# Kernel tuning notes

Measured on AMD Instinct MI355X. Metric: run time of the kernel, lower is better.

Reference implementation:

```python
import jax, jax.numpy as jnp
import numpy as np

C_LOGIT = 10.0  # logit clipping constant C from __init__
NEG_INF = -1e8


def setup_inputs() -> dict:
    key = jax.random.key(0)
    ks = jax.random.split(key, 10)
    B, S, E, H = 512, 256, 128, 128
    u = lambda k, sh: jax.random.uniform(k, sh, jnp.float32, -0.1, 0.1)
    return {
        "low_context_vector": jax.random.normal(ks[0], (B, S, E), jnp.float32),
        "original_node": jax.random.uniform(ks[1], (S, 2), jnp.float32),
        "mask": jnp.zeros((B, S), jnp.float32),
        # learned parameters
        "low_init_w": jax.random.uniform(ks[2], (2 * E,), jnp.float32, -1.0, 1.0),
        "Wc": u(ks[3], (E, E)),   "bc": u(ks[4], (E,)),     # low_h_context_embed
        "Wv": u(ks[5], (2 * E, E)), "bv": u(ks[6], (E,)),   # low_v_weight_embed
        "Wq": u(ks[7], (E, H)),                              # pointer query proj
        "Wref": u(ks[8], (E, H)),                            # pointer ref proj
        "v": u(ks[9], (H,)),                                 # pointer score vector
    }


def _decode(cv, mask, low_init_w, Wc, bc, Wv, bv, Wq, Wref, v, key):
    B, S, E = cv.shape
    h_bar = jnp.mean(cv, axis=1) @ Wc + bc              # [B,E]
    rest0 = low_init_w @ Wv + bv                        # [E]
    query0 = h_bar + rest0[None, :]                     # [B,E]
    ref = cv @ Wref                                     # [B,S,H], hoisted out of loop
    mask = mask.at[:, 0].set(1.0)                       # start node visited
    keys = jax.random.split(key, S - 1)
    binds = jnp.arange(B)

    def step(carry, k):
        mask, query, init_h, i = carry
        u_ = jnp.tanh((query @ Wq)[:, None, :] + ref) @ v      # [B,S]
        logits = jnp.where(mask > 0, NEG_INF, C_LOGIT * jnp.tanh(u_))
        logp = jax.nn.log_softmax(logits, axis=-1)
        g = jax.random.gumbel(k, logits.shape, logits.dtype)
        idx = jnp.argmax(logits + g, axis=-1)                  # Categorical sample, [B]
        lp = jnp.take_along_axis(logp, idx[:, None], axis=1)[:, 0]
        mask = mask.at[binds, idx].set(1.0)
        h = cv[binds, idx]                                     # gathered embedding [B,E]
        init_h = jnp.where(i == 0, h, init_h)                  # first pick cached
        query = h_bar + (jnp.concatenate([init_h, h], axis=-1) @ Wv + bv)
        return (mask, query, init_h, i + 1), (idx, lp)

    init = (mask, query0, jnp.zeros((B, E), cv.dtype), jnp.int32(0))
    _, (idxs, lps) = jax.lax.scan(step, init, keys)
    return idxs.T, lps.T  # [B, S-1] each


def reference(low_context_vector, original_node, mask, low_init_w, Wc, bc, Wv, bv, Wq, Wref, v):
    # original_node only feeds a printed local_reward in the torch code; it does
    # not affect the returned (indices, log_probs), so it is unused here.
    return _decode(low_context_vector, mask, low_init_w, Wc, bc, Wv, bv, Wq, Wref, v,
                   jax.random.key(42))
```

## Files before the change

### kernel.cpp

```cpp
#include <hip/hip_runtime.h>
#include <hip/hip_bf16.h>
#include <stdint.h>
#include <math.h>

#define NBATCH 512
#define NS 256
#define NE 128
#define NH 128
#define NSTEPS 255
#define NEGINF -1e8f
#define SENT_NEG -1e30f

__device__ __forceinline__ uint32_t rotl32(uint32_t x, uint32_t r) {
  return (x << r) | (x >> (32u - r));
}

__device__ __forceinline__ void tf2x32(uint32_t k0, uint32_t k1,
                                       uint32_t x0, uint32_t x1,
                                       uint32_t& o0, uint32_t& o1) {
  uint32_t ks2 = k0 ^ k1 ^ 0x1BD11BDAu;
  x0 += k0; x1 += k1;
#define TF_R4(a,b,c,d) \
  x0 += x1; x1 = rotl32(x1,a); x1 ^= x0; \
  x0 += x1; x1 = rotl32(x1,b); x1 ^= x0; \
  x0 += x1; x1 = rotl32(x1,c); x1 ^= x0; \
  x0 += x1; x1 = rotl32(x1,d); x1 ^= x0;
  TF_R4(13,15,26,6)   x0 += k1;  x1 += ks2 + 1u;
  TF_R4(17,29,16,24)  x0 += ks2; x1 += k0 + 2u;
  TF_R4(13,15,26,6)   x0 += k0;  x1 += k1 + 3u;
  TF_R4(17,29,16,24)  x0 += k1;  x1 += ks2 + 4u;
  TF_R4(13,15,26,6)   x0 += ks2; x1 += k0 + 5u;
#undef TF_R4
  o0 = x0; o1 = x1;
}

__device__ __forceinline__ float gumbel_of(uint2 key, uint32_t j) {
  uint32_t o0, o1;
  tf2x32(key.x, key.y, 0u, j, o0, o1);
  uint32_t bits = o0 ^ o1;
  float f = __uint_as_float((bits >> 9) | 0x3f800000u) - 1.0f;
  float u = (f == 0.0f) ? 1.17549435e-38f : f;
  float l1 = -logf(u);
  return -logf(l1);
}

__device__ __forceinline__ float nr_tanh(float x) {
  const float Chi = 2.8853900432586670f;
  const float Clo = 3.8519259822379735e-08f;
  float m = fmaf(x, Chi, x * Clo);
  m = fminf(m, 126.0f);
  float tt = __builtin_amdgcn_exp2f(m);
  float d  = tt + 1.0f;
  float r  = __builtin_amdgcn_rcpf(d);
  r = r * fmaf(-d, r, 2.0f);
  return fmaf(-2.0f, r, 1.0f);
}

__device__ __forceinline__ double dot32(const float4* __restrict__ a,
                                        const float4* __restrict__ bp) {
  double s = 0.0;
#pragma unroll
  for (int q = 0; q < 8; ++q) {
    float4 x = a[q], y = bp[q];
    s += (double)x.x * (double)y.x + (double)x.y * (double)y.y
       + (double)x.z * (double)y.z + (double)x.w * (double)y.w;
  }
  return s;
}

__device__ __forceinline__ double dot4d(float4 a, float4 b) {
  return ((double)a.x * (double)b.x + (double)a.y * (double)b.y)
       + ((double)a.z * (double)b.z + (double)a.w * (double)b.w);
}

__global__ void k1_mats(const float* __restrict__ Wv, const float* __restrict__ Wq,
                        const float* __restrict__ liw, const float* __restrict__ bvv,
                        float* __restrict__ M1T, float* __restrict__ M2T,
                        float* __restrict__ rest0) {
  int e = blockIdx.x, h = threadIdx.x;
  __shared__ float wrow[NE];
  if (e < 256) {
    wrow[h] = Wv[e * NE + h];
    __syncthreads();
    double a = 0.0;
    for (int k = 0; k < NE; ++k) a += (double)wrow[k] * (double)Wq[k * NH + h];
    if (e < 128) M1T[h * NE + e] = (float)a;
    else         M2T[h * NE + (e - 128)] = (float)a;
  } else {
    double a = 0.0;
    for (int k = 0; k < 2 * NE; ++k) a += (double)liw[k] * (double)Wv[k * NE + h];
    rest0[h] = (float)a + bvv[h];
  }
}

__global__ void k2_base(const float* __restrict__ cv, const float* __restrict__ Wc,
                        const float* __restrict__ bc, const float* __restrict__ bvv,
                        const float* __restrict__ Wq, const float* __restrict__ rest0,
                        double* __restrict__ qqbase, float* __restrict__ qq0) {
  int b = blockIdx.x, h = threadIdx.x;
  int b256 = b << 8;
  __shared__ float meanL[NE], hbarL[NE];
  double ms = 0.0;
  for (int s = 0; s < NS; ++s) ms += (double)cv[((size_t)b256 + s) * NE + h];
  meanL[h] = (float)(ms * (1.0 / 256.0));
  __syncthreads();
  double a = 0.0;
  for (int e = 0; e < NE; ++e) a += (double)meanL[e] * (double)Wc[e * NE + h];
  hbarL[h] = (float)a + bc[h];
  __syncthreads();
  double ab = 0.0, a0 = 0.0;
  for (int k = 0; k < NE; ++k) {
    double w = (double)Wq[k * NH + h];
    ab += (double)(hbarL[k] + bvv[k]) * w;
    a0 += (double)(hbarL[k] + rest0[k]) * w;
  }
  qqbase[(size_t)b * NH + h] = ab;
  qq0[(size_t)b * NH + h] = (float)a0;
}

__global__ __launch_bounds__(256, 4)
void k_a2v3(const float* __restrict__ cv, const float* __restrict__ M2T,
            double* __restrict__ A2) {
  const int b  = blockIdx.x >> 3;
  const int s0 = (blockIdx.x & 7) << 5;
  const int t  = threadIdx.x;
  const int h  = t >> 1;
  const int kh = t & 1;
  const int b256 = b << 8;
  __shared__ float cvS[32][132];
  for (int idx = t; idx < 32 * NE; idx += 256) {
    int r = idx >> 7, c = idx & 127;
    cvS[r][c] = cv[((size_t)(b256 + s0 + r)) * NE + c];
  }
  __syncthreads();
  float4 m2r[16];
  {
    const float4* m2p = (const float4*)(M2T + (size_t)h * NE + kh * 64);
#pragma unroll
    for (int q = 0; q < 16; ++q) m2r[q] = m2p[q];
  }
#pragma unroll 2
  for (int sLoc = 0; sLoc < 32; ++sLoc) {
    const float4* cr4 = ((const float4*)&cvS[sLoc][0]) + kh * 16;
    double c0 = 0.0, c1 = 0.0;
#pragma unroll
    for (int q = 0; q < 16; q += 2) {
      c0 += dot4d(cr4[q],     m2r[q]);
      c1 += dot4d(cr4[q + 1], m2r[q + 1]);
    }
    double s = c0 + c1;
    s += __shfl_xor(s, 1, 64);
    if (kh == 0)
      A2[((size_t)(b256 + s0 + sLoc)) * NH + h] = s;
  }
}

struct MainSh {
  alignas(16) float  qq[NH];
  alignas(16) float  vvf[NH];
  alignas(8)  double partA[NS];
  float  logitArr[NS];
  alignas(8)  double base128[NH];
  uint2  keyL[NSTEPS];
  float  redV[8];
  float  redS[8];
  int    redI[8];
};

struct PreSh {
  float cvS[NS][33];
  float wS[32][NH];
};

template <int MODE>
__global__ __launch_bounds__(512, 4)
void decode_main(const float* __restrict__ cv,
                 const float* __restrict__ mask_in,
                 const float* __restrict__ Wref,
                 const float* __restrict__ vvec,
                 const double* __restrict__ qqbase,
                 const float* __restrict__ M1T,
                 const float* __restrict__ M2T,
                 const float* __restrict__ qq0,
                 const double* __restrict__ A2,
                 float* __restrict__ out) {
  const int b = blockIdx.x;
  const int t = threadIdx.x;
  const int b256 = b << 8;
  const int chunk = (((t >> 6) & 3) + b) & 3;
  const int i = (chunk << 6) | (t & 63);
  const int halfo = t >> 8;
  const int hb = halfo << 6;

  __shared__ union { PreSh pre; MainSh m; } sh;
  __shared__ short rowIdA[NS], rowIdB[NS], posA[NS], posB[NS];
  __shared__ int nActSh[2], jSh[2], tmp8[4];
  __shared__ alignas(16) float refScratch[NE];

  bool act0 = false;
  if (t < NS) {
    act0 = !((t == 0) || (mask_in[(size_t)b256 + t] > 0.0f));
    uint64_t mb = __ballot(act0);
    int lane = t & 63, w = t >> 6;
    int pre = __popcll(mb & (((uint64_t)1 << lane) - 1));
    if (lane == 0) tmp8[w] = (int)__popcll(mb);
    posA[t] = (short)pre;
  }
  __syncthreads();
  if (t < NS) {
    int base = 0;
    for (int k = 0; k < (t >> 6); ++k) base += tmp8[k];
    int p = base + (int)posA[t];
    if (act0) rowIdA[p] = (short)t;
    posA[t] = (short)p;
  }
  if (t == 0) {
    nActSh[0] = tmp8[0] + tmp8[1] + tmp8[2] + tmp8[3];
    jSh[0] = -1;
  }
  __syncthreads();
  const int nAct0 = nActSh[0];

  const int myRow0 = (i < nAct0) ? (int)rowIdA[i] : 0;
  float refr[64];
#pragma unroll
  for (int j = 0; j < 64; ++j) refr[j] = 0.0f;

  for (int ec = 0; ec < 4; ++ec) {
    __syncthreads();
    for (int ii = t; ii < 32 * NH; ii += 512) {
      int r = ii >> 7, c = ii & 127;
      sh.pre.wS[r][c] = Wref[(ec * 32 + r) * NH + c];
    }
    for (int ii = t; ii < NS * 32; ii += 512) {
      int r = ii >> 5, c = ii & 31;
      sh.pre.cvS[r][c] = cv[((size_t)b256 + r) * NE + ec * 32 + c];
    }
    __syncthreads();
    for (int hc = 0; hc < 8; ++hc) {
      double a[8] = {0,0,0,0,0,0,0,0};
      for (int e = 0; e < 32; ++e) {
        double cd = (double)sh.pre.cvS[myRow0][e];
        const float* wp = &sh.pre.wS[e][hb + hc * 8];
#pragma unroll
        for (int j = 0; j < 8; ++j) a[j] += cd * (double)wp[j];
      }
#pragma unroll
      for (int j = 0; j < 8; ++j) refr[hc * 8 + j] += (float)a[j];
    }
  }
  __syncthreads();

  if (t < NSTEPS) {
    uint32_t o0, o1;
    tf2x32(0u, 42u, 0u, (uint32_t)t, o0, o1);
    sh.m.keyL[t] = make_uint2(o0, o1);
  }
  if (t < NH) {
    sh.m.vvf[t] = vvec[t];
    sh.m.qq[t] = qq0[(size_t)b * NH + t];
  }
  __syncthreads();

  float g = 0.0f;
  if (halfo && i < nAct0)
    g = gumbel_of(sh.m.keyL[0], (uint32_t)(b256 + myRow0));

  for (int step = 0; step < NSTEPS; ++step) {
    const int cur = step & 1;
    const short* rowId_c = cur ? rowIdB : rowIdA;
    const short* pos_c   = cur ? posB   : posA;
    short* rowId_n = cur ? rowIdA : rowIdB;
    short* pos_n   = cur ? posA   : posB;
    const int nA    = nActSh[cur];
    const int jPrev = jSh[cur];
    const bool active = (i < nA);
    const int myRow = active ? (int)rowId_c[i] : 0;

    if (jPrev >= 0 && i == jPrev) {
      const float4* rs4 = (const float4*)(refScratch + hb);
#pragma unroll
      for (int q = 0; q < 16; ++q) {
        float4 v4 = rs4[q];
        refr[4 * q + 0] = v4.x; refr[4 * q + 1] = v4.y;
        refr[4 * q + 2] = v4.z; refr[4 * q + 3] = v4.w;
      }
    }

    double accH = 0.0;
    if (active) {
      double a0 = 0, a1 = 0, a2 = 0, a3 = 0;
      const float4* qq4 = (const float4*)(sh.m.qq + hb);
      const float4* vv4 = (const float4*)(sh.m.vvf + hb);
#pragma unroll
      for (int q = 0; q < 16; ++q) {
        float4 qv = qq4[q];
        float4 wv = vv4[q];
        a0 += (double)nr_tanh(qv.x + refr[4 * q + 0]) * (double)wv.x;
        a1 += (double)nr_tanh(qv.y + refr[4 * q + 1]) * (double)wv.y;
        a2 += (double)nr_tanh(qv.z + refr[4 * q + 2]) * (double)wv.z;
        a3 += (double)nr_tanh(qv.w + refr[4 * q + 3]) * (double)wv.w;
      }
      accH = (a0 + a1) + (a2 + a3);
      if (!halfo) sh.m.partA[i] = accH;
    }
    __syncthreads();

    if (halfo) {
      float val = SENT_NEG; int vRow = 0x7fffffff; float term = 0.0f;
      if (active) {
        float u_ = (float)(sh.m.partA[i] + accH);
        float logit = 10.0f * (float)tanh((double)u_);
        sh.m.logitArr[myRow] = logit;
        term = expf(logit);
        val = logit + g;
        vRow = myRow;
      }
      float bvv = val; int bR = vRow; float bss = term;
#pragma unroll
      for (int mm = 1; mm <= 32; mm <<= 1) {
        float ov = __shfl_xor(bvv, mm, 64);
        int   oR = __shfl_xor(bR,  mm, 64);
        float os = __shfl_xor(bss, mm, 64);
        bss += os;
        if (ov > bvv || (ov == bvv && oR < bR)) { bvv = ov; bR = oR; }
      }
      if ((t & 63) == 0) {
        int w = t >> 6;
        sh.m.redV[w] = bvv; sh.m.redI[w] = bR; sh.m.redS[w] = bss;
      }
    }
    __syncthreads();

    float BV = sh.m.redV[4]; int BR = sh.m.redI[4];
#pragma unroll
    for (int k = 5; k < 8; ++k) {
      float ov = sh.m.redV[k]; int oR = sh.m.redI[k];
      if (ov > BV || (ov == BV && oR < BR)) { BV = ov; BR = oR; }
    }
    if ((unsigned)BR > 255u) BR = 0;
    const int BI = BR;
    const int jj = (int)pos_c[BI];

    double a2v = 0.0;
    if (MODE == 1 && step > 0 && step + 1 < NSTEPS && t < NH)
      a2v = A2[(size_t)(b256 + BI) * NH + t];

    if (t == 0) {
      float SS = (sh.m.redS[4] + sh.m.redS[5]) + (sh.m.redS[6] + sh.m.redS[7]);
      float lp = sh.m.logitArr[BI] - (float)log((double)SS);
      out[(size_t)b * NSTEPS + step] = (float)BI;
      out[(size_t)NBATCH * NSTEPS + (size_t)b * NSTEPS + step] = lp;
      nActSh[cur ^ 1] = nA - 1;
      jSh[cur ^ 1] = (jj < nA - 1) ? jj : -1;
    }

    if (t < NS) {
      int donorRow = (int)rowId_c[nA - 1];
      short rid = (t == jj) ? (short)donorRow : rowId_c[t];
      rowId_n[t] = rid;
      if (t < nA - 1) pos_n[rid] = (short)t;
    }
    if (jj < nA - 1 && i == nA - 1) {
      float4* rs4 = (float4*)(refScratch + hb);
#pragma unroll
      for (int q = 0; q < 16; ++q)
        rs4[q] = make_float4(refr[4 * q + 0], refr[4 * q + 1],
                             refr[4 * q + 2], refr[4 * q + 3]);
    }

    if (halfo && step + 1 < NSTEPS) {
      int nA_next = nA - 1;
      if (i < nA_next) {
        int ridN = (i == jj) ? (int)rowId_c[nA - 1] : myRow;
        g = gumbel_of(sh.m.keyL[step + 1], (uint32_t)(b256 + ridN));
      }
    }

    if (step + 1 < NSTEPS) {
      if (MODE == 1) {
        if (step == 0) {
          const int hq = t >> 2, kq = t & 3;
          const float4* hrow = (const float4*)(cv + (size_t)(b256 + BI) * NE + kq * 32);
          const float4* m1p  = (const float4*)(M1T + (size_t)hq * NE + kq * 32);
          double am = dot32(hrow, m1p);
          am += __shfl_xor(am, 1, 64);
          am += __shfl_xor(am, 2, 64);
          if (kq == 0) {
            double dbase = qqbase[(size_t)b * NH + hq] + am;
            sh.m.base128[hq] = dbase;
            sh.m.qq[hq] = (float)(dbase + A2[(size_t)(b256 + BI) * NH + hq]);
          }
        } else if (t < NH) {
          sh.m.qq[t] = (float)(sh.m.base128[t] + a2v);
        }
      } else {
        const int hq = t >> 2, kq = t & 3;
        const float4* hrow = (const float4*)(cv + (size_t)(b256 + BI) * NE + kq * 32);
        const float4* m2p  = (const float4*)(M2T + (size_t)hq * NE + kq * 32);
        double a2 = dot32(hrow, m2p);
        a2 += __shfl_xor(a2, 1, 64);
        a2 += __shfl_xor(a2, 2, 64);
        if (step == 0) {
          const float4* m1p = (const float4*)(M1T + (size_t)hq * NE + kq * 32);
          double am = dot32(hrow, m1p);
          am += __shfl_xor(am, 1, 64);
          am += __shfl_xor(am, 2, 64);
          if (kq == 0) {
            double dbase = qqbase[(size_t)b * NH + hq] + am;
            sh.m.base128[hq] = dbase;
            sh.m.qq[hq] = (float)(dbase + a2);
          }
        } else if (kq == 0) {
          sh.m.qq[hq] = (float)(sh.m.base128[hq] + a2);
        }
      }
    }
    __syncthreads();
  }
}

__device__ __forceinline__ float fast_tanh_ref(float x) {
  const float Chi = 2.8853900432586670f;
  const float Clo = 3.8519259822379735e-08f;
  float m = fmaf(x, Chi, x * Clo);
  float tt = exp2f(m);
  return 1.0f - 2.0f / (tt + 1.0f);
}

struct MainShR {
  float  query[NE];
  float  qq[NH];
  float  hbar[NE];
  float  inith[NE];
  float  hcur[NE];
  alignas(16) double vvd[NH];
  float  logitArr[NS];
  float  maskArr[NS];
  uint2  keyL[NSTEPS];
  float  meanv[NE];
  float  redV[4];
  int    redI[4];
  double redS[4];
  int    idxSh;
};
struct PreShR {
  float cvS[NS][33];
  float wS[32][NH];
};

__global__ __launch_bounds__(256, 2)
void decoder_kernel_ref(const float* __restrict__ cv, const float* __restrict__ mask_in,
                        const float* __restrict__ liw, const float* __restrict__ Wc,
                        const float* __restrict__ bc, const float* __restrict__ Wv,
                        const float* __restrict__ bv, const float* __restrict__ Wq,
                        const float* __restrict__ Wref, const float* __restrict__ vvec,
                        float* __restrict__ out) {
  const int b = blockIdx.x;
  const int t = threadIdx.x;
  const int b256 = b << 8;
  __shared__ union { PreShR pre; MainShR m; } sh;

  float refr[NH];
#pragma unroll
  for (int h = 0; h < NH; ++h) refr[h] = 0.0f;
  for (int ec = 0; ec < 4; ++ec) {
    const int e0 = ec * 32;
    __syncthreads();
    for (int i = t; i < 32 * NH; i += 256) {
      int r = i >> 7, h = i & 127;
      sh.pre.wS[r][h] = Wref[(e0 + r) * NH + h];
    }
    for (int i = t; i < NS * 32; i += 256) {
      int s2 = i >> 5, j = i & 31;
      sh.pre.cvS[s2][j] = cv[((size_t)b256 + s2) * NE + e0 + j];
    }
    __syncthreads();
#pragma unroll
    for (int hc = 0; hc < 16; ++hc) {
      double a[8] = {0,0,0,0,0,0,0,0};
      for (int e = 0; e < 32; ++e) {
        double cd = (double)sh.pre.cvS[t][e];
#pragma unroll
        for (int j = 0; j < 8; ++j) a[j] += cd * (double)sh.pre.wS[e][hc * 8 + j];
      }
#pragma unroll
      for (int j = 0; j < 8; ++j) refr[hc * 8 + j] += (float)a[j];
    }
  }
  __syncthreads();

  if (t < NSTEPS) {
    uint32_t o0, o1;
    tf2x32(0u, 42u, 0u, (uint32_t)t, o0, o1);
    sh.m.keyL[t] = make_uint2(o0, o1);
  }
  if (t < NH) sh.m.vvd[t] = (double)vvec[t];
  sh.m.maskArr[t] = (mask_in[(size_t)b256 + t] > 0.0f || t == 0) ? 1.0f : 0.0f;
  if (t < NE) {
    double s64 = 0.0;
    for (int s2 = 0; s2 < NS; ++s2) s64 += (double)cv[((size_t)b256 + s2) * NE + t];
    sh.m.meanv[t] = (float)(s64 * (1.0 / 256.0));
  }
  __syncthreads();
  if (t < NE) {
    double acc = 0.0;
    for (int e = 0; e < NE; ++e) acc += (double)sh.m.meanv[e] * (double)Wc[e * NE + t];
    float hbv = (float)acc + bc[t];
    sh.m.hbar[t] = hbv;
    double acc2 = 0.0;
    for (int k = 0; k < 2 * NE; ++k) acc2 += (double)liw[k] * (double)Wv[k * NE + t];
    float r0 = (float)acc2 + bv[t];
    sh.m.query[t] = hbv + r0;
  }
  __syncthreads();

  for (int step = 0; step < NSTEPS; ++step) {
    if (t < NH) {
      double acc = 0.0;
      for (int k = 0; k < NE; ++k) acc += (double)sh.m.query[k] * (double)Wq[k * NH + t];
      sh.m.qq[t] = (float)acc;
    }
    __syncthreads();

    float logit;
    bool masked = (sh.m.maskArr[t] != 0.0f);
    if (!masked) {
      double a0 = 0.0, a1 = 0.0, a2 = 0.0, a3 = 0.0;
      const float4*  qq4 = (const float4*)sh.m.qq;
      const double2* vv2 = (const double2*)sh.m.vvd;
#pragma unroll
      for (int h4 = 0; h4 < 32; ++h4) {
        float4  q  = qq4[h4];
        double2 va = vv2[2 * h4];
        double2 vb = vv2[2 * h4 + 1];
        a0 += (double)fast_tanh_ref(q.x + refr[4 * h4 + 0]) * va.x;
        a1 += (double)fast_tanh_ref(q.y + refr[4 * h4 + 1]) * va.y;
        a2 += (double)fast_tanh_ref(q.z + refr[4 * h4 + 2]) * vb.x;
        a3 += (double)fast_tanh_ref(q.w + refr[4 * h4 + 3]) * vb.y;
      }
      float u_ = (float)((a0 + a1) + (a2 + a3));
      logit = 10.0f * (float)tanh((double)u_);
    } else {
      logit = NEGINF;
    }
    sh.m.logitArr[t] = logit;

    uint2 key = sh.m.keyL[step];
    uint32_t j = (uint32_t)(b256 + t);
    uint32_t o0, o1;
    tf2x32(key.x, key.y, 0u, j, o0, o1);
    uint32_t bits = o0 ^ o1;
    float f = __uint_as_float((bits >> 9) | 0x3f800000u) - 1.0f;
    float u = (f == 0.0f) ? 1.17549435e-38f : f;
    float l1 = (float)(-log((double)u));
    float g  = (float)(-log((double)l1));
    float val = logit + g;
    double term = exp((double)logit);

    float bv_ = val; int bi = t; double bs = term;
#pragma unroll
    for (int m = 1; m <= 32; m <<= 1) {
      float  ov = __shfl_xor(bv_, m, 64);
      int    oi = __shfl_xor(bi,  m, 64);
      double os = __shfl_xor(bs,  m, 64);
      if (ov > bv_ || (ov == bv_ && oi < bi)) { bv_ = ov; bi = oi; }
      bs += os;
    }
    int w = t >> 6;
    if ((t & 63) == 0) { sh.m.redV[w] = bv_; sh.m.redI[w] = bi; sh.m.redS[w] = bs; }
    __syncthreads();

    if (t == 0) {
      float BV = sh.m.redV[0]; int BI = sh.m.redI[0];
      for (int k = 1; k < 4; ++k) {
        float ov = sh.m.redV[k]; int oi = sh.m.redI[k];
        if (ov > BV || (ov == BV && oi < BI)) { BV = ov; BI = oi; }
      }
      double SS = ((sh.m.redS[0] + sh.m.redS[1]) + (sh.m.redS[2] + sh.m.redS[3]));
      sh.m.idxSh = BI;
      float lp = sh.m.logitArr[BI] - (float)log(SS);
      out[(size_t)b * NSTEPS + step] = (float)BI;
      out[(size_t)NBATCH * NSTEPS + (size_t)b * NSTEPS + step] = lp;
    }
    __syncthreads();

    int idx = sh.m.idxSh;
    if (t == idx) sh.m.maskArr[t] = 1.0f;
    if (t < NE) {
      float hc = cv[((size_t)b256 + idx) * NE + t];
      sh.m.hcur[t] = hc;
      if (step == 0) sh.m.inith[t] = hc;
    }
    __syncthreads();

    if (t < NE) {
      double acc2 = 0.0;
      for (int k = 0; k < NE; ++k) acc2 += (double)sh.m.inith[k] * (double)Wv[k * NE + t];
      for (int k = 0; k < NE; ++k) acc2 += (double)sh.m.hcur[k] * (double)Wv[(NE + k) * NE + t];
      float mm = (float)acc2 + bv[t];
      sh.m.query[t] = sh.m.hbar[t] + mm;
    }
    __syncthreads();
  }
}

extern "C" void kernel_launch(void* const* d_in, const int* in_sizes, int n_in,
                              void* d_out, int out_size, void* d_ws, size_t ws_size,
                              hipStream_t stream) {
  const float* cv   = (const float*)d_in[0];
  const float* mask = (const float*)d_in[2];
  const float* liw  = (const float*)d_in[3];
  const float* Wc   = (const float*)d_in[4];
  const float* bc   = (const float*)d_in[5];
  const float* Wv   = (const float*)d_in[6];
  const float* bv   = (const float*)d_in[7];
  const float* Wq   = (const float*)d_in[8];
  const float* Wref = (const float*)d_in[9];
  const float* vv   = (const float*)d_in[10];
  (void)in_sizes; (void)n_in; (void)out_size;

  const size_t SZ_QQB = (size_t)NBATCH * NH * sizeof(double);
  const size_t SZ_M   = (size_t)NE * NH * sizeof(float);
  const size_t SZ_QQ0 = (size_t)NBATCH * NH * sizeof(float);
  const size_t SZ_A2  = (size_t)NBATCH * NS * NH * sizeof(double);
  const size_t need_min = SZ_QQB + 2 * SZ_M + SZ_QQ0 + 512;
  const size_t need_pre = need_min + SZ_A2;

  if (ws_size >= need_min) {
    char* p = (char*)d_ws;
    double* qqbase = (double*)p;            p += SZ_QQB;
    float*  M1T    = (float*)p;             p += SZ_M;
    float*  M2T    = (float*)p;             p += SZ_M;
    float*  qq0    = (float*)p;             p += SZ_QQ0;
    float*  rest0  = (float*)p;             p += 512;
    double* A2     = (double*)p;

    k1_mats<<<257, 128, 0, stream>>>(Wv, Wq, liw, bv, M1T, M2T, rest0);
    k2_base<<<NBATCH, 128, 0, stream>>>(cv, Wc, bc, bv, Wq, rest0, qqbase, qq0);
    if (ws_size >= need_pre) {
      k_a2v3<<<NBATCH * 8, 256, 0, stream>>>(cv, M2T, A2);
      decode_main<1><<<NBATCH, 512, 0, stream>>>(cv, mask, Wref, vv, qqbase, M1T,
                                                 M2T, qq0, A2, (float*)d_out);
    } else {
      decode_main<0><<<NBATCH, 512, 0, stream>>>(cv, mask, Wref, vv, qqbase, M1T,
                                                 M2T, qq0, nullptr, (float*)d_out);
    }
  } else {
    decoder_kernel_ref<<<NBATCH, 256, 0, stream>>>(cv, mask, liw, Wc, bc, Wv, bv,
                                                   Wq, Wref, vv, (float*)d_out);
  }
}
```

Baseline: 3.163 ms.

## Pair H-halves in adjacent lanes to drop a barrier and prefetch A2 row

```diff
diff --git a/kernel.cpp b/kernel.cpp
--- a/kernel.cpp
+++ b/kernel.cpp
@@ -158,7 +158,6 @@
 struct MainSh {
   alignas(16) float  qq[NH];
   alignas(16) float  vvf[NH];
-  alignas(8)  double partA[NS];
   float  logitArr[NS];
   alignas(8)  double base128[NH];
   uint2  keyL[NSTEPS];
@@ -187,10 +186,10 @@
   const int b = blockIdx.x;
   const int t = threadIdx.x;
   const int b256 = b << 8;
-  const int chunk = (((t >> 6) & 3) + b) & 3;
-  const int i = (chunk << 6) | (t & 63);
-  const int halfo = t >> 8;
-  const int hb = halfo << 6;
+  const int w = t >> 6, l = t & 63;
+  const int i = (w << 5) | (l >> 1);
+  const int hHalf = l & 1;
+  const int hb = hHalf << 6;
 
   __shared__ union { PreSh pre; MainSh m; } sh;
   __shared__ short rowIdA[NS], rowIdB[NS], posA[NS], posB[NS];
@@ -201,9 +200,9 @@
   if (t < NS) {
     act0 = !((t == 0) || (mask_in[(size_t)b256 + t] > 0.0f));
     uint64_t mb = __ballot(act0);
-    int lane = t & 63, w = t >> 6;
+    int lane = t & 63, wv = t >> 6;
     int pre = __popcll(mb & (((uint64_t)1 << lane) - 1));
-    if (lane == 0) tmp8[w] = (int)__popcll(mb);
+    if (lane == 0) tmp8[wv] = (int)__popcll(mb);
     posA[t] = (short)pre;
   }
   __syncthreads();
@@ -263,7 +262,7 @@
   __syncthreads();
 
   float g = 0.0f;
-  if (halfo && i < nAct0)
+  if (i < nAct0)
     g = gumbel_of(sh.m.keyL[0], (uint32_t)(b256 + myRow0));
 
   for (int step = 0; step < NSTEPS; ++step) {
@@ -302,39 +301,45 @@
         a3 += (double)nr_tanh(qv.w + refr[4 * q + 3]) * (double)wv.w;
       }
       accH = (a0 + a1) + (a2 + a3);
-      if (!halfo) sh.m.partA[i] = accH;
-    }
-    __syncthreads();
-
-    if (halfo) {
-      float val = SENT_NEG; int vRow = 0x7fffffff; float term = 0.0f;
-      if (active) {
-        float u_ = (float)(sh.m.partA[i] + accH);
-        float logit = 10.0f * (float)tanh((double)u_);
+    }
+    double other = __shfl_xor(accH, 1, 64);
+    float val = SENT_NEG; int vRow = 0x7fffffff; float term = 0.0f;
+    if (active) {
+      double tot = hHalf ? (other + accH) : (accH + other);
+      float u_ = (float)tot;
+      float logit = 10.0f * (float)tanh((double)u_);
+      if (!hHalf) {
         sh.m.logitArr[myRow] = logit;
         term = expf(logit);
-        val = logit + g;
-        vRow = myRow;
-      }
-      float bvv = val; int bR = vRow; float bss = term;
-#pragma unroll
-      for (int mm = 1; mm <= 32; mm <<= 1) {
-        float ov = __shfl_xor(bvv, mm, 64);
-        int   oR = __shfl_xor(bR,  mm, 64);
-        float os = __shfl_xor(bss, mm, 64);
-        bss += os;
-        if (ov > bvv || (ov == bvv && oR < bR)) { bvv = ov; bR = oR; }
-      }
-      if ((t & 63) == 0) {
-        int w = t >> 6;
-        sh.m.redV[w] = bvv; sh.m.redI[w] = bR; sh.m.redS[w] = bss;
-      }
-    }
-    __syncthreads();
-
-    float BV = sh.m.redV[4]; int BR = sh.m.redI[4];
-#pragma unroll
-    for (int k = 5; k < 8; ++k) {
+      }
+      val = logit + g;
+      vRow = myRow;
+    }
+
+    float bvv = val; int bR = vRow; float bss = term;
+#pragma unroll
+    for (int mm = 1; mm <= 32; mm <<= 1) {
+      float ov = __shfl_xor(bvv, mm, 64);
+      int   oR = __shfl_xor(bR,  mm, 64);
+      float os = __shfl_xor(bss, mm, 64);
+      bss += os;
+      if (ov > bvv || (ov == bvv && oR < bR)) { bvv = ov; bR = oR; }
+    }
+
+    double pf0 = 0.0, pf1 = 0.0;
+    bool havePf = false;
+    if (MODE == 1 && step > 0 && step + 1 < NSTEPS && (unsigned)bR <= 255u) {
+      const double* ap = A2 + (size_t)(b256 + bR) * NH + (l << 1);
+      pf0 = ap[0]; pf1 = ap[1];
+      havePf = true;
+    }
+
+    if (l == 0) { sh.m.redV[w] = bvv; sh.m.redI[w] = bR; sh.m.redS[w] = bss; }
+    __syncthreads();
+
+    float BV = sh.m.redV[0]; int BR = sh.m.redI[0];
+#pragma unroll
+    for (int k = 1; k < 8; ++k) {
       float ov = sh.m.redV[k]; int oR = sh.m.redI[k];
       if (ov > BV || (ov == BV && oR < BR)) { BV = ov; BR = oR; }
     }
@@ -342,12 +347,9 @@
     const int BI = BR;
     const int jj = (int)pos_c[BI];
 
-    double a2v = 0.0;
-    if (MODE == 1 && step > 0 && step + 1 < NSTEPS && t < NH)
-      a2v = A2[(size_t)(b256 + BI) * NH + t];
-
     if (t == 0) {
-      float SS = (sh.m.redS[4] + sh.m.redS[5]) + (sh.m.redS[6] + sh.m.redS[7]);
+      float SS = (sh.m.redS[0] + sh.m.redS[1]) + (sh.m.redS[2] + sh.m.redS[3]);
+      SS += (sh.m.redS[4] + sh.m.redS[5]) + (sh.m.redS[6] + sh.m.redS[7]);
       float lp = sh.m.logitArr[BI] - (float)log((double)SS);
       out[(size_t)b * NSTEPS + step] = (float)BI;
       out[(size_t)NBATCH * NSTEPS + (size_t)b * NSTEPS + step] = lp;
@@ -369,12 +371,9 @@
                              refr[4 * q + 2], refr[4 * q + 3]);
     }
 
-    if (halfo && step + 1 < NSTEPS) {
-      int nA_next = nA - 1;
-      if (i < nA_next) {
-        int ridN = (i == jj) ? (int)rowId_c[nA - 1] : myRow;
-        g = gumbel_of(sh.m.keyL[step + 1], (uint32_t)(b256 + ridN));
-      }
+    if (step + 1 < NSTEPS && i < nA - 1) {
+      int ridN = (i == jj) ? (int)rowId_c[nA - 1] : myRow;
+      g = gumbel_of(sh.m.keyL[step + 1], (uint32_t)(b256 + ridN));
     }
 
     if (step + 1 < NSTEPS) {
@@ -391,8 +390,10 @@
             sh.m.base128[hq] = dbase;
             sh.m.qq[hq] = (float)(dbase + A2[(size_t)(b256 + BI) * NH + hq]);
           }
-        } else if (t < NH) {
-          sh.m.qq[t] = (float)(sh.m.base128[t] + a2v);
+        } else if (havePf && bR == BI) {
+          const int h0 = l << 1;
+          sh.m.qq[h0]     = (float)(sh.m.base128[h0]     + pf0);
+          sh.m.qq[h0 + 1] = (float)(sh.m.base128[h0 + 1] + pf1);
         }
       } else {
         const int hq = t >> 2, kq = t & 3;
```

New measurement: 3.029 ms. 1.04x faster.
